# Performance work log

Hardware: AMD Instinct MI355X
Metric: run time of the kernel (lower is better)

## Reference

```python
import jax, jax.numpy as jnp
import numpy as np

B, S, H = 8, 2048, 1024

def setup_inputs() -> dict:
    key = jax.random.key(0)
    k1, k2 = jax.random.split(key)
    inputs = jax.random.normal(k1, (B, S, H), dtype=jnp.float32)
    # PyTorch Linear weight [out, in]; init ~ U(-1/sqrt(H), 1/sqrt(H)) approximated with scaled normal
    W = jax.random.normal(k2, (H, H), dtype=jnp.float32) * (1.0 / np.sqrt(H))
    b = jnp.zeros((H,), dtype=jnp.float32)
    return {"inputs": inputs, "W": W, "b": b}

def reference(inputs, W, b):
    # QW = inputs @ W^T + b   (nn.Linear)
    QW = jnp.einsum('bsh,oh->bso', inputs, W) + b  # [B,S,H]
    # score = QW @ inputs^T  (no scaling, no mask)
    score = jnp.einsum('bqh,bkh->bqk', QW, inputs)  # [B,S,S]
    attn = jax.nn.softmax(score, axis=2)
    # output = attn @ inputs
    output = jnp.einsum('bqk,bkh->bqh', attn, inputs)  # [B,S,H]
    return output
```

## Files before the change

kernel.cpp:

```cpp
#include <hip/hip_runtime.h>
#include <hip/hip_bf16.h>
#include <hip/hip_fp16.h>

typedef unsigned short u16;
typedef __attribute__((ext_vector_type(8))) _Float16 f16x8;
typedef __attribute__((ext_vector_type(4))) float f32x4;

#define B_ 8
#define S_ 2048
#define H_ 1024
#define M_ (B_ * S_)

__device__ __forceinline__ u16 f2h(float f) {
  _Float16 h = (_Float16)f;
  return __builtin_bit_cast(u16, h);
}

__global__ void f32_to_f16_kernel(const float* __restrict__ x,
                                  u16* __restrict__ o, int n4) {
  int stride = gridDim.x * blockDim.x;
  for (int i = blockIdx.x * blockDim.x + threadIdx.x; i < n4; i += stride) {
    float4 v = reinterpret_cast<const float4*>(x)[i];
    ushort4 h;
    h.x = f2h(v.x); h.y = f2h(v.y); h.z = f2h(v.z); h.w = f2h(v.w);
    reinterpret_cast<ushort4*>(o)[i] = h;
  }
}

__global__ void transpose_f32_kernel(const float* __restrict__ x,
                                     u16* __restrict__ xt,
                                     u16* __restrict__ xf) {
  __shared__ u16 t[64][65];
  int b = blockIdx.z, s0 = blockIdx.x * 64, h0 = blockIdx.y * 64;
  int tx = threadIdx.x, ty = threadIdx.y;
  const float* src = x + ((size_t)b * S_ + s0) * H_ + h0;
  u16* dstf = xf + ((size_t)b * S_ + s0) * H_ + h0;
#pragma unroll
  for (int i = 0; i < 4; ++i) {
    u16 h = f2h(src[(size_t)(ty + 16 * i) * H_ + tx]);
    t[ty + 16 * i][tx] = h;
    dstf[(size_t)(ty + 16 * i) * H_ + tx] = h;
  }
  __syncthreads();
  u16* dst = xt + ((size_t)b * H_ + h0) * S_ + s0;
#pragma unroll
  for (int i = 0; i < 4; ++i)
    dst[(size_t)(ty + 16 * i) * S_ + tx] = t[tx][ty + 16 * i];
}

__device__ __forceinline__ void async_stage16(const u16* g, u16* l) {
  __builtin_amdgcn_global_load_lds(
      (__attribute__((address_space(1))) void*)g,
      (__attribute__((address_space(3))) void*)l, 16, 0, 0);
}

template <int OM>
__global__ __launch_bounds__(512) void gemm8_kernel(
    const u16* __restrict__ A, const u16* __restrict__ B,
    float* __restrict__ Cf, u16* __restrict__ Ch,
    const float* __restrict__ bias,
    int lda, int ldb, int ldc, int K,
    long sAz, long sBz, long sCz) {
  __shared__ __align__(16) u16 sA[2][256 * 64];
  __shared__ __align__(16) u16 sB[2][256 * 64];

  int gx = gridDim.x, gy = gridDim.y;
  int nwg = gx * gy * gridDim.z;
  int wgid = blockIdx.x + gx * (blockIdx.y + gy * blockIdx.z);
  int q = nwg >> 3, r = nwg & 7;
  int xcd = wgid & 7, idx = wgid >> 3;
  int nid = (xcd < r ? xcd * (q + 1) : r * (q + 1) + (xcd - r) * q) + idx;
  int bxi = nid % gx, t2 = nid / gx;
  int byi = t2 % gy, bzi = t2 / gy;

  int tid = threadIdx.x, wave = tid >> 6, lane = tid & 63;
  int wm = wave >> 2, wn = wave & 3;
  int bm = bxi * 256, bn = byi * 256;
  long zA = (long)bzi * sAz;
  long zB = (long)bzi * sBz;
  long zC = (long)bzi * sCz;
  const u16* gA = A + zA + (size_t)bm * lda;
  const u16* gB = B + zB + (size_t)bn * ldb;

  int srow = tid >> 3;
  int scolb = (tid & 7) << 4;
  int sco = (scolb ^ ((srow & 7) << 4)) >> 1;
  size_t aO0 = (size_t)srow * lda + sco, aO1 = aO0 + (size_t)64 * lda;
  size_t bO0 = (size_t)srow * ldb + sco, bO1 = bO0 + (size_t)64 * ldb;
  int ld0 = srow * 64 + (scolb >> 1), ld1 = ld0 + 64 * 64;

  auto stgA = [&](int slot, int half, int kofs) {
    const u16* g = gA + (size_t)(half * 128) * lda + kofs;
    u16* l = &sA[slot][half * 8192];
    async_stage16(g + aO0, l + ld0);
    async_stage16(g + aO1, l + ld1);
  };
  auto stgB = [&](int slot, int half, int kofs) {
    const u16* g = gB + (size_t)(half * 128) * ldb + kofs;
    u16* l = &sB[slot][half * 8192];
    async_stage16(g + bO0, l + ld0);
    async_stage16(g + bO1, l + ld1);
  };

  int la = lane & 15;
  int kg = (lane >> 4) << 4;
  auto frag = [&](const u16* base, int row, int colb) -> f16x8 {
    int off = (row << 7) + (colb ^ ((row & 7) << 4));
    return *reinterpret_cast<const f16x8*>(
        reinterpret_cast<const char*>(base) + off);
  };

  f16x8 aF[4][2], bF[2][2];
  f32x4 acc[8][4] = {};

  auto RA = [&](int slot, int qm) {
#pragma unroll
    for (int j = 0; j < 4; ++j)
#pragma unroll
      for (int ks = 0; ks < 2; ++ks)
        aF[j][ks] = frag(sA[slot], qm * 128 + (j * 2 + wm) * 16 + la,
                         ks * 64 + kg);
  };
  auto RB = [&](int slot, int qn) {
#pragma unroll
    for (int i = 0; i < 2; ++i)
#pragma unroll
      for (int ks = 0; ks < 2; ++ks)
        bF[i][ks] = frag(sB[slot], qn * 128 + (i * 4 + wn) * 16 + la,
                         ks * 64 + kg);
  };
  auto MM = [&](int qm, int qn) {
#pragma unroll
    for (int ks = 0; ks < 2; ++ks)
#pragma unroll
      for (int j = 0; j < 4; ++j)
#pragma unroll
        for (int i = 0; i < 2; ++i)
          acc[qm * 4 + j][qn * 2 + i] = __builtin_amdgcn_mfma_f32_16x16x32_f16(
              aF[j][ks], bF[i][ks], acc[qm * 4 + j][qn * 2 + i], 0, 0, 0);
  };

#define VM4 asm volatile("s_waitcnt vmcnt(4)" ::: "memory")
#define VM2 asm volatile("s_waitcnt vmcnt(2)" ::: "memory")
#define VM0 asm volatile("s_waitcnt vmcnt(0)" ::: "memory")
#define LG8 asm volatile("s_waitcnt lgkmcnt(8)" ::: "memory")
#define BAR __builtin_amdgcn_s_barrier()
#define LG0                                              \
  asm volatile("s_waitcnt lgkmcnt(0)" ::: "memory");     \
  __builtin_amdgcn_sched_barrier(0)
#define MFMA_CL(qm, qn)                 \
  __builtin_amdgcn_s_setprio(1);        \
  MM(qm, qn);                           \
  __builtin_amdgcn_s_setprio(0)

  stgA(0, 0, 0); stgB(0, 0, 0); stgB(0, 1, 0); stgA(0, 1, 0);
  VM4;
  BAR;

  int NT = K >> 6;
  for (int t = 0; t < NT; ++t) {
    int s = t & 1, ns = s ^ 1;
    int kn = (t + 1) << 6;
    bool more = (t + 1 < NT);
    RA(s, 0); RB(s, 0);
    if (more) stgA(ns, 0, kn);
    LG8;
    BAR; LG0; MFMA_CL(0, 0);
    if (more) { VM4; } else { VM2; }
    BAR;
    RB(s, 1);
    if (more) stgB(ns, 0, kn);
    BAR; LG0; MFMA_CL(0, 1);
    if (more) { VM4; } else { VM0; }
    BAR;
    RA(s, 1);
    if (more) stgB(ns, 1, kn);
    BAR; LG0; MFMA_CL(1, 1);
    BAR;
    RB(s, 0);
    if (more) stgA(ns, 1, kn);
    BAR; LG0; MFMA_CL(1, 0);
    if (more) { VM4; }
    BAR;
  }
#undef VM4
#undef VM2
#undef VM0
#undef LG8
#undef BAR
#undef LG0
#undef MFMA_CL

#pragma unroll
  for (int mf = 0; mf < 8; ++mf) {
    int qm = mf >> 2, j = mf & 3;
    int row = bm + qm * 128 + (j * 2 + wm) * 16 + (lane >> 4) * 4;
#pragma unroll
    for (int nf = 0; nf < 4; ++nf) {
      int qn = nf >> 1, i = nf & 1;
      int col = bn + qn * 128 + (i * 4 + wn) * 16 + la;
#pragma unroll
      for (int r = 0; r < 4; ++r) {
        float v = acc[mf][nf][r];
        if constexpr (OM == 1) {
          Ch[zC + (size_t)(row + r) * ldc + col] = f2h(v + bias[col]);
        } else {
          Cf[zC + (size_t)(row + r) * ldc + col] = v;
        }
      }
    }
  }
}

__global__ __launch_bounds__(256) void softmax_kernel(const float* __restrict__ sc,
                                                      u16* __restrict__ attn,
                                                      int opitch) {
  __shared__ float red[4];
  size_t row = blockIdx.x;
  const float* p = sc + row * S_;
  u16* o = attn + row * (size_t)opitch;
  int t = threadIdx.x;
  float4 v0 = reinterpret_cast<const float4*>(p)[t];
  float4 v1 = reinterpret_cast<const float4*>(p)[t + 256];
  float mx = fmaxf(fmaxf(fmaxf(v0.x, v0.y), fmaxf(v0.z, v0.w)),
                   fmaxf(fmaxf(v1.x, v1.y), fmaxf(v1.z, v1.w)));
#pragma unroll
  for (int d = 32; d > 0; d >>= 1) mx = fmaxf(mx, __shfl_xor(mx, d));
  if ((t & 63) == 0) red[t >> 6] = mx;
  __syncthreads();
  mx = fmaxf(fmaxf(red[0], red[1]), fmaxf(red[2], red[3]));
  float e[8];
  e[0] = __expf(v0.x - mx); e[1] = __expf(v0.y - mx);
  e[2] = __expf(v0.z - mx); e[3] = __expf(v0.w - mx);
  e[4] = __expf(v1.x - mx); e[5] = __expf(v1.y - mx);
  e[6] = __expf(v1.z - mx); e[7] = __expf(v1.w - mx);
  float s = ((e[0] + e[1]) + (e[2] + e[3])) + ((e[4] + e[5]) + (e[6] + e[7]));
#pragma unroll
  for (int d = 32; d > 0; d >>= 1) s += __shfl_xor(s, d);
  __syncthreads();
  if ((t & 63) == 0) red[t >> 6] = s;
  __syncthreads();
  s = (red[0] + red[1]) + (red[2] + red[3]);
  float inv = 1.0f / s;
  ushort4 h0, h1;
  h0.x = f2h(e[0] * inv); h0.y = f2h(e[1] * inv);
  h0.z = f2h(e[2] * inv); h0.w = f2h(e[3] * inv);
  h1.x = f2h(e[4] * inv); h1.y = f2h(e[5] * inv);
  h1.z = f2h(e[6] * inv); h1.w = f2h(e[7] * inv);
  reinterpret_cast<ushort4*>(o)[t] = h0;
  reinterpret_cast<ushort4*>(o)[t + 256] = h1;
}

extern "C" void kernel_launch(void* const* d_in, const int* in_sizes, int n_in,
                              void* d_out, int out_size, void* d_ws, size_t ws_size,
                              hipStream_t stream) {
  const float* X = (const float*)d_in[0];
  const float* W = (const float*)d_in[1];
  const float* bias = (const float*)d_in[2];
  float* out = (float*)d_out;
  char* ws = (char*)d_ws;

  const size_t MB = 1ull << 20;
  u16* XF = (u16*)(ws);
  u16* WF = (u16*)(ws + 32 * MB);
  u16* XT = (u16*)(ws + 34 * MB);
  u16* QW = (u16*)(ws + 66 * MB);
  float* SC = (float*)(ws + 98 * MB);
  u16* PF = (u16*)(ws + 162 * MB);

  int plan = (ws_size >= 226 * MB) ? 2 : (ws_size >= 163 * MB) ? 1 : 0;
  int CB = (plan >= 1) ? 4 : 2;
  int nch = B_ / CB;

  f32_to_f16_kernel<<<1024, 256, 0, stream>>>(W, WF, H_ * H_ / 4);
  transpose_f32_kernel<<<dim3(S_ / 64, H_ / 64, B_), dim3(64, 16), 0, stream>>>(
      X, XT, XF);
  gemm8_kernel<1><<<dim3(M_ / 256, H_ / 256, 1), 512, 0, stream>>>(
      XF, WF, nullptr, QW, bias, H_, H_, H_, H_, 0, 0, 0);
  for (int ch = 0; ch < nch; ++ch) {
    long off = (long)ch * CB;
    gemm8_kernel<0><<<dim3(S_ / 256, S_ / 256, CB), 512, 0, stream>>>(
        QW + off * S_ * H_, XF + off * S_ * H_, SC, nullptr, nullptr,
        H_, H_, S_, H_, (long)S_ * H_, (long)S_ * H_, (long)S_ * S_);
    if (plan == 2) {
      softmax_kernel<<<CB * S_, 256, 0, stream>>>(
          SC, PF + off * S_ * S_, S_);
    } else {
      softmax_kernel<<<CB * S_, 256, 0, stream>>>(
          SC, (u16*)SC, 2 * S_);
      gemm8_kernel<0><<<dim3(S_ / 256, H_ / 256, CB), 512, 0, stream>>>(
          (u16*)SC, XT + off * (long)H_ * S_,
          out + off * (long)S_ * H_, nullptr, nullptr,
          2 * S_, S_, H_, S_, (long)S_ * 2 * S_, (long)H_ * S_, (long)S_ * H_);
    }
  }
  if (plan == 2) {
    gemm8_kernel<0><<<dim3(S_ / 256, H_ / 256, B_), 512, 0, stream>>>(
        PF, XT, out, nullptr, nullptr,
        S_, S_, H_, S_, (long)S_ * S_, (long)H_ * S_, (long)S_ * H_);
  }
}
```

Before: 265.6 us.

## Deepen GEMM global-to-LDS prefetch to two k-tiles ahead

Restructures the double-buffered MFMA GEMM main loop so global-to-LDS staging is issued up to two k-tiles ahead. Three of the four quarter-tiles for step t+2 are written into the current slot right after they are read, and one quarter for t+1 is staged at the start of each iteration. The vmcnt waits change from per-quarter waits of 4/2 to a single wait of 6 per iteration, with a vmcnt(0) drain on the second-to-last step. This is meant to hide more global load latency, at the cost of tricky slot-reuse ordering and more loads in flight.

```diff
diff --git a/kernel.cpp b/kernel.cpp
--- a/kernel.cpp
+++ b/kernel.cpp
@@ -140,8 +140,7 @@
               aF[j][ks], bF[i][ks], acc[qm * 4 + j][qn * 2 + i], 0, 0, 0);
   };
 
-#define VM4 asm volatile("s_waitcnt vmcnt(4)" ::: "memory")
-#define VM2 asm volatile("s_waitcnt vmcnt(2)" ::: "memory")
+#define VM6 asm volatile("s_waitcnt vmcnt(6)" ::: "memory")
 #define VM0 asm volatile("s_waitcnt vmcnt(0)" ::: "memory")
 #define LG8 asm volatile("s_waitcnt lgkmcnt(8)" ::: "memory")
 #define BAR __builtin_amdgcn_s_barrier()
@@ -153,38 +152,32 @@
   MM(qm, qn);                           \
   __builtin_amdgcn_s_setprio(0)
 
+  int NT = K >> 6;
   stgA(0, 0, 0); stgB(0, 0, 0); stgB(0, 1, 0); stgA(0, 1, 0);
-  VM4;
+  if (NT > 1) { stgA(1, 0, 64); stgB(1, 1, 64); stgA(1, 1, 64); }
+  VM6;
   BAR;
 
-  int NT = K >> 6;
   for (int t = 0; t < NT; ++t) {
     int s = t & 1, ns = s ^ 1;
-    int kn = (t + 1) << 6;
-    bool more = (t + 1 < NT);
+    int k1 = (t + 1) << 6, k2 = (t + 2) << 6;
+    bool p1 = (t + 1 < NT), p2 = (t + 2 < NT);
     RA(s, 0); RB(s, 0);
-    if (more) stgA(ns, 0, kn);
+    if (p1) stgB(ns, 0, k1);
     LG8;
-    BAR; LG0; MFMA_CL(0, 0);
-    if (more) { VM4; } else { VM2; }
-    BAR;
+    BAR; LG0; MFMA_CL(0, 0); BAR;
     RB(s, 1);
-    if (more) stgB(ns, 0, kn);
-    BAR; LG0; MFMA_CL(0, 1);
-    if (more) { VM4; } else { VM0; }
-    BAR;
+    if (p2) stgA(s, 0, k2);
+    BAR; LG0; MFMA_CL(0, 1); BAR;
     RA(s, 1);
-    if (more) stgB(ns, 1, kn);
-    BAR; LG0; MFMA_CL(1, 1);
-    BAR;
+    if (p2) stgB(s, 1, k2);
+    BAR; LG0; MFMA_CL(1, 1); BAR;
     RB(s, 0);
-    if (more) stgA(ns, 1, kn);
-    BAR; LG0; MFMA_CL(1, 0);
-    if (more) { VM4; }
-    BAR;
-  }
-#undef VM4
-#undef VM2
+    if (p2) stgA(s, 1, k2);
+    if (t < NT - 2) { VM6; } else if (t == NT - 2) { VM0; }
+    BAR; LG0; MFMA_CL(1, 0); BAR;
+  }
+#undef VM6
 #undef VM0
 #undef LG8
 #undef BAR
```

After: 257.3 us. 1.03x faster.
